# Performance work log

Hardware: AMD Instinct MI355X
Metric: run time of the kernel (lower is better)

Reference implementation:

```python
import jax, jax.numpy as jnp
import numpy as np

B, DZ, DS, DH = 8192, 1024, 64, 4096

def setup_inputs() -> dict:
    key = jax.random.key(0)
    ks = jax.random.split(key, 8)
    r1 = 1.0 / np.sqrt(DZ)   # W1 init range (last dim dz)
    r2 = 1.0 / np.sqrt(DH)   # W2 init range (last dim dim_hidden)
    rc = 1.0 / np.sqrt(DS)   # C init range
    return {
        "z": jax.random.normal(ks[0], (B, DZ), jnp.float32),
        "s": jax.random.normal(ks[1], (B, DS), jnp.float32),
        "A": jnp.full((DZ,), 0.95, jnp.float32),
        "W1": jax.random.uniform(ks[2], (DH, DZ), jnp.float32, -r1, r1),
        "W2": jax.random.uniform(ks[3], (DZ, DH), jnp.float32, -r2, r2),
        "h1": jax.random.normal(ks[4], (DH,), jnp.float32),
        "h2": jax.random.normal(ks[5], (DZ,), jnp.float32),
        "C": jax.random.uniform(ks[6], (DZ, DS), jnp.float32, -rc, rc),
    }

def reference(z, s, A, W1, W2, h1, h2, C):
    # PLRNN step, W_trial=False, mean_center=False, noise=0:
    # z' = A*z + relu(z @ W1.T + h1) @ W2.T + h2 + s @ C.T
    z_activated = jax.nn.relu(z @ W1.T + h1)          # [B, DH]
    return A * z + z_activated @ W2.T + h2 + s @ C.T  # [B, DZ]
```

## Files before the change

### kernel.cpp

```cpp
#include <hip/hip_runtime.h>

#define BB 8192
#define DZ 1024
#define DS 64
#define DH 4096
#define KEXT (DH + DS)

typedef float floatx4 __attribute__((ext_vector_type(4)));
typedef __bf16 bf16x8 __attribute__((ext_vector_type(8)));
typedef __bf16 bf16x4 __attribute__((ext_vector_type(4)));
typedef __attribute__((address_space(1))) void* as1_void_ptr;
typedef __attribute__((address_space(3))) void* as3_void_ptr;

#define WAIT_VM0   3952
#define WAIT_VM8   3960
#define WAIT_LGKM0 49279

__device__ __forceinline__ void async_copy16(const void* g, void* l) {
    __builtin_amdgcn_global_load_lds((as1_void_ptr)g, (as3_void_ptr)l, 16, 0, 0);
}

__device__ __forceinline__ bf16x4 cvt4(float4 v) {
    bf16x4 o = { (__bf16)v.x, (__bf16)v.y, (__bf16)v.z, (__bf16)v.w };
    return o;
}

__device__ __forceinline__ bf16x8 cvt8(float4 a, float4 b) {
    bf16x8 o = { (__bf16)a.x, (__bf16)a.y, (__bf16)a.z, (__bf16)a.w,
                 (__bf16)b.x, (__bf16)b.y, (__bf16)b.z, (__bf16)b.w };
    return o;
}


__global__ __launch_bounds__(256) void prep_all(
    const float* __restrict__ z, const float* __restrict__ W1,
    const float* __restrict__ W2, const float* __restrict__ C,
    const float* __restrict__ s,
    __bf16* __restrict__ zb, __bf16* __restrict__ W1b,
    __bf16* __restrict__ B2b, __bf16* __restrict__ Hb)
{
    constexpr int NC_Z  = (BB * DZ) / 8;
    constexpr int NC_W1 = (DH * DZ) / 8;
    constexpr int NC_B2 = (DZ * KEXT) / 8;
    constexpr int NC_S  = (BB * DS) / 8;
    constexpr int NC_TOT = NC_Z + NC_W1 + NC_B2 + NC_S;
    const int stride = gridDim.x * blockDim.x;
    for (int c = blockIdx.x * blockDim.x + threadIdx.x; c < NC_TOT; c += stride) {
        const float4* src;
        __bf16* dst;
        if (c < NC_Z) {
            src = (const float4*)z + (size_t)c * 2;
            dst = zb + (size_t)c * 8;
        } else if (c < NC_Z + NC_W1) {
            int i = c - NC_Z;
            src = (const float4*)W1 + (size_t)i * 2;
            dst = W1b + (size_t)i * 8;
        } else if (c < NC_Z + NC_W1 + NC_B2) {
            int i = c - (NC_Z + NC_W1);
            int j = i / 520, p = i - j * 520;
            int h = p * 8;
            const float* sp = (h < DH) ? (W2 + (size_t)j * DH + h)
                                       : (C  + (size_t)j * DS + (h - DH));
            src = (const float4*)sp;
            dst = B2b + (size_t)j * KEXT + h;
        } else {
            int i = c - (NC_Z + NC_W1 + NC_B2);
            int r = i >> 3, k = (i & 7) * 8;
            src = (const float4*)(s + (size_t)r * DS + k);
            dst = Hb + (size_t)r * KEXT + DH + k;
        }
        float4 a = src[0], b = src[1];
        *(bf16x8*)dst = cvt8(a, b);
    }
}

__global__ __launch_bounds__(512, 4) void gemm1_relu(
    const __bf16* __restrict__ Ag, const __bf16* __restrict__ Bg,
    const float* __restrict__ h1, __bf16* __restrict__ Hb)
{
    constexpr int ldA = DZ, ldB = DZ, KITER = DZ / 64;
    __shared__ __align__(16) __bf16 As[256 * 64];
    __shared__ __align__(16) __bf16 Bs[128 * 64];

    const int tid = threadIdx.x;
    const int wave = tid >> 6, lane = tid & 63;
    const int wm = wave >> 1, wn = wave & 1;
    const int row0 = blockIdx.x * 256;
    const int col0 = blockIdx.y * 128;

    const int csrc = ((tid & 3) ^ ((tid >> 3) & 3)) * 8;
    const __bf16* pA = Ag + (size_t)(row0 + (tid >> 2)) * ldA + csrc;
    const __bf16* pB = Bg + (size_t)(col0 + ((tid >> 2) & 127)) * ldB + csrc;
    __bf16* lA = As + wave * 512;
    __bf16* lB = Bs + wave * 512;

    const int cswz = ((lane >> 4) ^ ((lane >> 1) & 3)) * 8;
    const __bf16* Afrag = As + (wm * 64 + (lane & 15)) * 32 + cswz;
    const __bf16* Bfrag = Bs + (wn * 64 + (lane & 15)) * 32 + cswz;

    floatx4 acc[4][4];
#pragma unroll
    for (int i = 0; i < 4; ++i)
#pragma unroll
        for (int j = 0; j < 4; ++j) acc[i][j] = (floatx4)0.0f;

    for (int kt = 0; kt < KITER; ++kt) {
        const __bf16* ak = pA + kt * 64;
        const __bf16* bk = pB + kt * 64;
        async_copy16(ak,                           lA);
        async_copy16(ak + (size_t)128 * ldA,       lA + 4096);
        async_copy16(ak + 32,                      lA + 8192);
        async_copy16(ak + (size_t)128 * ldA + 32,  lA + 8192 + 4096);
        async_copy16(bk,                           lB);
        async_copy16(bk + 32,                      lB + 4096);
        __builtin_amdgcn_s_waitcnt(0);
        __syncthreads();

#pragma unroll
        for (int ks = 0; ks < 2; ++ks) {
            bf16x8 af[4], bfr[4];
#pragma unroll
            for (int i = 0; i < 4; ++i) af[i] = *(const bf16x8*)(Afrag + ks * 8192 + i * 16 * 32);
#pragma unroll
            for (int j = 0; j < 4; ++j) bfr[j] = *(const bf16x8*)(Bfrag + ks * 4096 + j * 16 * 32);
#pragma unroll
            for (int i = 0; i < 4; ++i)
#pragma unroll
                for (int j = 0; j < 4; ++j)
                    acc[i][j] = __builtin_amdgcn_mfma_f32_16x16x32_bf16(af[i], bfr[j], acc[i][j], 0, 0, 0);
        }
        __syncthreads();
    }

    const int r0 = row0 + wm * 64 + (lane >> 4) * 4;
    const int c0 = col0 + wn * 64 + (lane & 15);
#pragma unroll
    for (int i = 0; i < 4; ++i) {
#pragma unroll
        for (int j = 0; j < 4; ++j) {
            int c = c0 + j * 16;
            float bias = h1[c];
#pragma unroll
            for (int rg = 0; rg < 4; ++rg) {
                int r = r0 + i * 16 + rg;
                float v = acc[i][j][rg] + bias;
                v = v > 0.0f ? v : 0.0f;
                Hb[(size_t)r * KEXT + c] = (__bf16)v;
            }
        }
    }
}

__global__ __launch_bounds__(256, 2) void gemm2_out(
    const __bf16* __restrict__ Ag, const __bf16* __restrict__ Bg,
    const float* __restrict__ Adiag, const float* __restrict__ h2,
    const float* __restrict__ z, float* __restrict__ out)
{
    constexpr int ldA = KEXT, ldB = KEXT, KITER = KEXT / 64;
    __shared__ __align__(16) __bf16 As[2 * 128 * 64];
    __shared__ __align__(16) __bf16 Bs[2 * 128 * 64];

    const int tid = threadIdx.x;
    const int wave = tid >> 6, lane = tid & 63;
    const int wm = wave >> 1, wn = wave & 1;
    const int row0 = blockIdx.x * 128;
    const int col0 = blockIdx.y * 128;

    const int csrc = ((tid & 3) ^ ((tid >> 3) & 3)) * 8;
    const __bf16* pA = Ag + (size_t)(row0 + (tid >> 2)) * ldA + csrc;
    const __bf16* pB = Bg + (size_t)(col0 + (tid >> 2)) * ldB + csrc;

    const int cswz = ((lane >> 4) ^ ((lane >> 1) & 3)) * 8;
    const __bf16* Afrag = As + (wm * 64 + (lane & 15)) * 32 + cswz;
    const __bf16* Bfrag = Bs + (wn * 64 + (lane & 15)) * 32 + cswz;

    floatx4 acc[4][4];
#pragma unroll
    for (int i = 0; i < 4; ++i)
#pragma unroll
        for (int j = 0; j < 4; ++j) acc[i][j] = (floatx4)0.0f;

    auto issue = [&](int kt, int q) {
        const __bf16* ak = pA + kt * 64;
        const __bf16* bk = pB + kt * 64;
        __bf16* lA = As + q * 8192 + wave * 512;
        __bf16* lB = Bs + q * 8192 + wave * 512;
        async_copy16(ak,                          lA);
        async_copy16(ak + (size_t)64 * ldA,       lA + 2048);
        async_copy16(ak + 32,                     lA + 4096);
        async_copy16(ak + (size_t)64 * ldA + 32,  lA + 4096 + 2048);
        async_copy16(bk,                          lB);
        async_copy16(bk + (size_t)64 * ldB,       lB + 2048);
        async_copy16(bk + 32,                     lB + 4096);
        async_copy16(bk + (size_t)64 * ldB + 32,  lB + 4096 + 2048);
    };

    issue(0, 0);

    for (int kt = 0; kt < KITER; ++kt) {
        const int p = kt & 1;
        if (kt + 1 < KITER) {
            issue(kt + 1, p ^ 1);
            __builtin_amdgcn_s_waitcnt(WAIT_VM8);
        } else {
            __builtin_amdgcn_s_waitcnt(WAIT_VM0);
        }
        __builtin_amdgcn_s_barrier();

#pragma unroll
        for (int ks = 0; ks < 2; ++ks) {
            const __bf16* Ab = Afrag + p * 8192 + ks * 4096;
            const __bf16* Bb = Bfrag + p * 8192 + ks * 4096;
            bf16x8 af[4], bfr[4];
#pragma unroll
            for (int i = 0; i < 4; ++i) af[i] = *(const bf16x8*)(Ab + i * 16 * 32);
#pragma unroll
            for (int j = 0; j < 4; ++j) bfr[j] = *(const bf16x8*)(Bb + j * 16 * 32);
#pragma unroll
            for (int i = 0; i < 4; ++i)
#pragma unroll
                for (int j = 0; j < 4; ++j)
                    acc[i][j] = __builtin_amdgcn_mfma_f32_16x16x32_bf16(af[i], bfr[j], acc[i][j], 0, 0, 0);
        }

        __builtin_amdgcn_s_waitcnt(WAIT_LGKM0);
        __builtin_amdgcn_s_barrier();
    }

    const int r0 = row0 + wm * 64 + (lane >> 4) * 4;
    const int c0 = col0 + wn * 64 + (lane & 15);
#pragma unroll
    for (int i = 0; i < 4; ++i) {
#pragma unroll
        for (int j = 0; j < 4; ++j) {
            const int c = c0 + j * 16;
            const float aj = Adiag[c];
            const float hj = h2[c];
#pragma unroll
            for (int rg = 0; rg < 4; ++rg) {
                const int r = r0 + i * 16 + rg;
                out[(size_t)r * DZ + c] =
                    acc[i][j][rg] + aj * z[(size_t)r * DZ + c] + hj;
            }
        }
    }
}


extern "C" void kernel_launch(void* const* d_in, const int* in_sizes, int n_in,
                              void* d_out, int out_size, void* d_ws, size_t ws_size,
                              hipStream_t stream) {
    const float* z  = (const float*)d_in[0];
    const float* s  = (const float*)d_in[1];
    const float* A  = (const float*)d_in[2];
    const float* W1 = (const float*)d_in[3];
    const float* W2 = (const float*)d_in[4];
    const float* h1 = (const float*)d_in[5];
    const float* h2 = (const float*)d_in[6];
    const float* C  = (const float*)d_in[7];
    float* out = (float*)d_out;

    char* ws = (char*)d_ws;
    size_t offHb  = 0;
    size_t offZb  = offHb  + (size_t)BB * KEXT * 2;
    size_t offW1b = offZb  + (size_t)BB * DZ * 2;
    size_t offB2b = offW1b + (size_t)DH * DZ * 2;
    __bf16* Hb  = (__bf16*)(ws + offHb);
    __bf16* zb  = (__bf16*)(ws + offZb);
    __bf16* W1b = (__bf16*)(ws + offW1b);
    __bf16* B2b = (__bf16*)(ws + offB2b);

    prep_all<<<2048, 256, 0, stream>>>(z, W1, W2, C, s, zb, W1b, B2b, Hb);
    gemm1_relu<<<dim3(BB / 256, DH / 128), 512, 0, stream>>>(zb, W1b, h1, Hb);
    gemm2_out<<<dim3(BB / 128, DZ / 128), 256, 0, stream>>>(Hb, B2b, A, h2, z, out);
}
```

Baseline: 250.8 us.

## Enlarge gemm1 tile to 256x256 with double-buffered async LDS pipeline

The first GEMM kernel moves from a 256x128 tile with a single LDS buffer and full waitcnt/sync per k-step to a 256x256 tile with double-buffered half-k stages. Global-to-LDS loads are issued one phase ahead and interleaved with MFMA phases using fine-grained vmcnt waits, barriers and setprio. The intent is to hide global load latency and raise arithmetic intensity per block. In exchange it uses more LDS and registers (128 accumulators per lane) with occupancy bounds lowered to 2, and launches half as many blocks.

```diff
diff --git a/kernel.cpp b/kernel.cpp
--- a/kernel.cpp
+++ b/kernel.cpp
@@ -13,16 +13,12 @@
 typedef __attribute__((address_space(3))) void* as3_void_ptr;
 
 #define WAIT_VM0   3952
+#define WAIT_VM4   3956
 #define WAIT_VM8   3960
 #define WAIT_LGKM0 49279
 
 __device__ __forceinline__ void async_copy16(const void* g, void* l) {
     __builtin_amdgcn_global_load_lds((as1_void_ptr)g, (as3_void_ptr)l, 16, 0, 0);
-}
-
-__device__ __forceinline__ bf16x4 cvt4(float4 v) {
-    bf16x4 o = { (__bf16)v.x, (__bf16)v.y, (__bf16)v.z, (__bf16)v.w };
-    return o;
 }
 
 __device__ __forceinline__ bf16x8 cvt8(float4 a, float4 b) {
@@ -74,68 +70,104 @@
     }
 }
 
-__global__ __launch_bounds__(512, 4) void gemm1_relu(
+#define G1_PH(Q, KS, IH, STAGE_STMT, WVM) do {                                 \
+    const __bf16* Ab_ = Afrag + (Q)*16384 + (KS)*8192 + (IH)*2048;             \
+    bf16x8 af_[4];                                                             \
+    _Pragma("unroll")                                                          \
+    for (int i_ = 0; i_ < 4; ++i_) af_[i_] = *(const bf16x8*)(Ab_ + i_*512);   \
+    if ((IH) == 0) {                                                           \
+        const __bf16* Bb_ = Bfrag + (Q)*16384 + (KS)*8192;                     \
+        _Pragma("unroll")                                                      \
+        for (int j_ = 0; j_ < 4; ++j_) bfr[j_] = *(const bf16x8*)(Bb_ + j_*512);\
+    }                                                                          \
+    STAGE_STMT;                                                                \
+    __builtin_amdgcn_s_barrier();                                              \
+    __builtin_amdgcn_s_waitcnt(WAIT_LGKM0);                                    \
+    __builtin_amdgcn_s_setprio(1);                                             \
+    _Pragma("unroll")                                                          \
+    for (int i_ = 0; i_ < 4; ++i_)                                             \
+        _Pragma("unroll")                                                      \
+        for (int j_ = 0; j_ < 4; ++j_)                                         \
+            acc[(IH)*4+i_][j_] = __builtin_amdgcn_mfma_f32_16x16x32_bf16(      \
+                af_[i_], bfr[j_], acc[(IH)*4+i_][j_], 0, 0, 0);                \
+    __builtin_amdgcn_s_setprio(0);                                             \
+    if ((WVM) >= 0) __builtin_amdgcn_s_waitcnt(WVM);                           \
+    __builtin_amdgcn_s_barrier();                                              \
+} while (0)
+
+__global__ __launch_bounds__(512, 2) void gemm1_relu(
     const __bf16* __restrict__ Ag, const __bf16* __restrict__ Bg,
     const float* __restrict__ h1, __bf16* __restrict__ Hb)
 {
     constexpr int ldA = DZ, ldB = DZ, KITER = DZ / 64;
-    __shared__ __align__(16) __bf16 As[256 * 64];
-    __shared__ __align__(16) __bf16 Bs[128 * 64];
+    __shared__ __align__(16) __bf16 As[2 * 2 * 256 * 32];
+    __shared__ __align__(16) __bf16 Bs[2 * 2 * 256 * 32];
 
     const int tid = threadIdx.x;
     const int wave = tid >> 6, lane = tid & 63;
-    const int wm = wave >> 1, wn = wave & 1;
+    const int wm = wave >> 2, wn = wave & 3;
     const int row0 = blockIdx.x * 256;
-    const int col0 = blockIdx.y * 128;
+    const int col0 = blockIdx.y * 256;
 
     const int csrc = ((tid & 3) ^ ((tid >> 3) & 3)) * 8;
     const __bf16* pA = Ag + (size_t)(row0 + (tid >> 2)) * ldA + csrc;
-    const __bf16* pB = Bg + (size_t)(col0 + ((tid >> 2) & 127)) * ldB + csrc;
-    __bf16* lA = As + wave * 512;
-    __bf16* lB = Bs + wave * 512;
+    const __bf16* pB = Bg + (size_t)(col0 + (tid >> 2)) * ldB + csrc;
 
     const int cswz = ((lane >> 4) ^ ((lane >> 1) & 3)) * 8;
-    const __bf16* Afrag = As + (wm * 64 + (lane & 15)) * 32 + cswz;
-    const __bf16* Bfrag = Bs + (wn * 64 + (lane & 15)) * 32 + cswz;
-
-    floatx4 acc[4][4];
-#pragma unroll
-    for (int i = 0; i < 4; ++i)
+    const __bf16* Afrag = As + (wm * 128 + (lane & 15)) * 32 + cswz;
+    const __bf16* Bfrag = Bs + (wn * 64  + (lane & 15)) * 32 + cswz;
+
+    auto sA0 = [&](int t, int q) { const __bf16* a = pA + t * 64;
+        __bf16* d = As + q * 16384 + wave * 512;
+        async_copy16(a, d); async_copy16(a + (size_t)128 * ldA, d + 4096); };
+    auto sB0 = [&](int t, int q) { const __bf16* b = pB + t * 64;
+        __bf16* d = Bs + q * 16384 + wave * 512;
+        async_copy16(b, d); async_copy16(b + (size_t)128 * ldB, d + 4096); };
+    auto sA1 = [&](int t, int q) { const __bf16* a = pA + t * 64 + 32;
+        __bf16* d = As + q * 16384 + 8192 + wave * 512;
+        async_copy16(a, d); async_copy16(a + (size_t)128 * ldA, d + 4096); };
+    auto sB1 = [&](int t, int q) { const __bf16* b = pB + t * 64 + 32;
+        __bf16* d = Bs + q * 16384 + 8192 + wave * 512;
+        async_copy16(b, d); async_copy16(b + (size_t)128 * ldB, d + 4096); };
+
+    floatx4 acc[8][4];
+#pragma unroll
+    for (int i = 0; i < 8; ++i)
 #pragma unroll
         for (int j = 0; j < 4; ++j) acc[i][j] = (floatx4)0.0f;
-
-    for (int kt = 0; kt < KITER; ++kt) {
-        const __bf16* ak = pA + kt * 64;
-        const __bf16* bk = pB + kt * 64;
-        async_copy16(ak,                           lA);
-        async_copy16(ak + (size_t)128 * ldA,       lA + 4096);
-        async_copy16(ak + 32,                      lA + 8192);
-        async_copy16(ak + (size_t)128 * ldA + 32,  lA + 8192 + 4096);
-        async_copy16(bk,                           lB);
-        async_copy16(bk + 32,                      lB + 4096);
-        __builtin_amdgcn_s_waitcnt(0);
-        __syncthreads();
-
-#pragma unroll
-        for (int ks = 0; ks < 2; ++ks) {
-            bf16x8 af[4], bfr[4];
-#pragma unroll
-            for (int i = 0; i < 4; ++i) af[i] = *(const bf16x8*)(Afrag + ks * 8192 + i * 16 * 32);
-#pragma unroll
-            for (int j = 0; j < 4; ++j) bfr[j] = *(const bf16x8*)(Bfrag + ks * 4096 + j * 16 * 32);
-#pragma unroll
-            for (int i = 0; i < 4; ++i)
-#pragma unroll
-                for (int j = 0; j < 4; ++j)
-                    acc[i][j] = __builtin_amdgcn_mfma_f32_16x16x32_bf16(af[i], bfr[j], acc[i][j], 0, 0, 0);
-        }
-        __syncthreads();
-    }
-
-    const int r0 = row0 + wm * 64 + (lane >> 4) * 4;
+    bf16x8 bfr[4];
+
+    sA0(0, 0); sB0(0, 0); sA1(0, 0); sB1(0, 0);
+    sA0(1, 1); sB0(1, 1);
+    __builtin_amdgcn_s_waitcnt(WAIT_VM8);
+    __builtin_amdgcn_s_barrier();
+
+    for (int r = 0; r < KITER / 2 - 1; ++r) {
+        const int t1 = 2 * r + 1, t2 = 2 * r + 2, t3 = 2 * r + 3;
+        G1_PH(0, 0, 0, sA1(t1, 1), -1);
+        G1_PH(0, 0, 1, sB1(t1, 1), WAIT_VM8);
+        G1_PH(0, 1, 0, sA0(t2, 0), -1);
+        G1_PH(0, 1, 1, sB0(t2, 0), WAIT_VM8);
+        G1_PH(1, 0, 0, sA1(t2, 0), -1);
+        G1_PH(1, 0, 1, sB1(t2, 0), WAIT_VM8);
+        G1_PH(1, 1, 0, sA0(t3, 1), -1);
+        G1_PH(1, 1, 1, sB0(t3, 1), WAIT_VM8);
+    }
+    {
+        G1_PH(0, 0, 0, sA1(15, 1), -1);
+        G1_PH(0, 0, 1, sB1(15, 1), WAIT_VM8);
+        G1_PH(0, 1, 0, (void)0,    -1);
+        G1_PH(0, 1, 1, (void)0,    WAIT_VM4);
+        G1_PH(1, 0, 0, (void)0,    -1);
+        G1_PH(1, 0, 1, (void)0,    WAIT_VM0);
+        G1_PH(1, 1, 0, (void)0,    -1);
+        G1_PH(1, 1, 1, (void)0,    -1);
+    }
+
+    const int r0 = row0 + wm * 128 + (lane >> 4) * 4;
     const int c0 = col0 + wn * 64 + (lane & 15);
 #pragma unroll
-    for (int i = 0; i < 4; ++i) {
+    for (int i = 0; i < 8; ++i) {
 #pragma unroll
         for (int j = 0; j < 4; ++j) {
             int c = c0 + j * 16;
@@ -271,6 +303,6 @@
     __bf16* B2b = (__bf16*)(ws + offB2b);
 
     prep_all<<<2048, 256, 0, stream>>>(z, W1, W2, C, s, zb, W1b, B2b, Hb);
-    gemm1_relu<<<dim3(BB / 256, DH / 128), 512, 0, stream>>>(zb, W1b, h1, Hb);
+    gemm1_relu<<<dim3(BB / 256, DH / 256), 512, 0, stream>>>(zb, W1b, h1, Hb);
     gemm2_out<<<dim3(BB / 128, DZ / 128), 256, 0, stream>>>(Hb, B2b, A, h2, z, out);
 }
```

After: 266.7 us. +6.3%, slower.
